# Kernel optimization log

Measured on AMD Instinct MI355X. Metric: run time of the kernel, lower is better.

Reference implementation:

```python
import jax, jax.numpy as jnp
import numpy as np

N = 100000          # num nodes
E = 1600000         # num edges (before self-loops)
IN = 128            # in_channels
HID = 32            # hidden_channels (= per-head dim, concat=False)
HEADS = 4
NEG_SLOPE = 0.2     # PyG GATConv default


def _glorot(k, shape):
    fan = shape[0] + shape[-1]
    return jax.random.normal(k, shape, jnp.float32) * np.float32(np.sqrt(2.0 / fan))


def setup_inputs() -> dict:
    key = jax.random.key(0)
    ks = jax.random.split(key, 18)
    inp = {}
    inp['x'] = jax.random.normal(ks[0], (N, IN), jnp.float32)
    inp['edge_index'] = jax.random.randint(ks[1], (2, E), 0, N, dtype=jnp.int64)
    dims_in = [IN, HID, HID]
    for i in range(3):
        inp[f'W{i+1}'] = _glorot(ks[2 + 4 * i], (dims_in[i], HEADS * HID))
        inp[f'as{i+1}'] = _glorot(ks[3 + 4 * i], (HEADS, HID))
        inp[f'ad{i+1}'] = _glorot(ks[4 + 4 * i], (HEADS, HID))
        inp[f'b{i+1}'] = jnp.zeros((HID,), jnp.float32)
    inp['lw1'] = _glorot(ks[14], (HID, HID // 2))
    inp['lb1'] = jnp.zeros((HID // 2,), jnp.float32)
    inp['lw2'] = _glorot(ks[15], (HID // 2, 1))
    inp['lb2'] = jnp.zeros((1,), jnp.float32)
    return inp


def gat_conv(x, src, dst, W, a_s, a_d, b):
    # x: [N, F_in]; src/dst: [E'] (self-loops included); concat=False -> head mean
    n = x.shape[0]
    h = (x @ W).reshape(n, HEADS, HID)                      # [N, H, C]
    alpha_src = jnp.einsum('nhc,hc->nh', h, a_s)            # [N, H]
    alpha_dst = jnp.einsum('nhc,hc->nh', h, a_d)            # [N, H]
    e = jax.nn.leaky_relu(alpha_src[src] + alpha_dst[dst], NEG_SLOPE)  # [E', H]
    # softmax over edges grouped by destination node
    e_max = jax.ops.segment_max(e, dst, num_segments=n)     # [N, H]
    e = jnp.exp(e - e_max[dst])
    denom = jax.ops.segment_sum(e, dst, num_segments=n)     # [N, H]
    alpha = e / (denom[dst] + 1e-16)                        # [E', H]
    msg = h[src] * alpha[:, :, None]                        # [E', H, C]
    out = jax.ops.segment_sum(msg, dst, num_segments=n)     # [N, H, C]
    return out.mean(axis=1) + b                             # concat=False: mean heads


def reference(x, edge_index, W1, as1, ad1, b1, W2, as2, ad2, b2, W3, as3, ad3, b3, lw1, lb1, lw2, lb2):
    # add self-loops (PyG GATConv default add_self_loops=True)
    loop = jnp.arange(N, dtype=edge_index.dtype)
    src = jnp.concatenate([edge_index[0], loop])
    dst = jnp.concatenate([edge_index[1], loop])
    h = jax.nn.relu(gat_conv(x, src, dst, W1, as1, ad1, b1))
    h = jax.nn.relu(gat_conv(h, src, dst, W2, as2, ad2, b2))
    h = jax.nn.relu(gat_conv(h, src, dst, W3, as3, ad3, b3))
    g = h.mean(axis=0, keepdims=True)                       # global_mean_pool, batch=None -> [1, HID]
    g = jax.nn.relu(g @ lw1 + lb1)                          # dropout is identity in eval
    return g @ lw2 + lb2                                    # [1, 1]
```

## Files before the change

### kernel.cpp

```cpp
#include <hip/hip_runtime.h>
#include <hip/hip_bf16.h>


#define HEADS 4
#define HID 32
#define F_HID 128
#define NEG_SLOPE 0.2f
#define BSHIFT 5
#define MAXB 3328
#define CAP 768
#define NSCAT 256

typedef float v2f __attribute__((ext_vector_type(2)));
using s8bf  = __attribute__((ext_vector_type(8))) short;
using f32x4 = __attribute__((ext_vector_type(4))) float;

__device__ __forceinline__ float lrelu(float v) { return v > 0.f ? v : NEG_SLOPE * v; }

__device__ __forceinline__ uint32_t bf16_rne(float f) {
    union { float f; uint32_t u; } c; c.f = f;
    return (c.u + 0x7fffu + ((c.u >> 16) & 1u)) >> 16;
}
__device__ __forceinline__ v2f up2(uint32_t u) {
    v2f r;
    r.x = __uint_as_float(u << 16);
    r.y = __uint_as_float(u & 0xffff0000u);
    return r;
}
__device__ __forceinline__ float bperm_f(int addr, float v) {
    return __int_as_float(__builtin_amdgcn_ds_bpermute(addr, __float_as_int(v)));
}
__device__ __forceinline__ int bperm_i(int addr, int v) {
    return __builtin_amdgcn_ds_bpermute(addr, v);
}
__device__ __forceinline__ v2f vshflxor(v2f v, int m) {
    v2f r; r.x = __shfl_xor(v.x, m); r.y = __shfl_xor(v.y, m); return r;
}


__device__ __forceinline__ void prep_one(const float* W, const float* a_s, const float* a_d,
                                         unsigned short* wbt, int FIN, int idx) {
    int LDK = FIN + 8;
    int r = idx / LDK, k = idx % LDK;
    float v = 0.f;
    if (k < FIN) {
        if (r < 128) {
            v = W[(size_t)k * F_HID + r];
        } else if (r < 136) {
            int j = r - 128;
            const float* av = (j < 4) ? a_s : a_d;
            int hd = j & 3;
            float s = 0.f;
            for (int c = 0; c < 32; c++)
                s += W[(size_t)k * F_HID + hd * 32 + c] * av[hd * 32 + c];
            v = s;
        }
    }
    wbt[idx] = (unsigned short)bf16_rne(v);
}

__global__ __launch_bounds__(256) void prep_all(const float* __restrict__ W1, const float* __restrict__ as1, const float* __restrict__ ad1,
                                                const float* __restrict__ W2, const float* __restrict__ as2, const float* __restrict__ ad2,
                                                const float* __restrict__ W3, const float* __restrict__ as3, const float* __restrict__ ad3,
                                                unsigned short* __restrict__ wbt1,
                                                unsigned short* __restrict__ wbt2,
                                                unsigned short* __restrict__ wbt3,
                                                int* __restrict__ gcursor, int nb,
                                                float* __restrict__ g) {
    int t = blockIdx.x * 256 + threadIdx.x;
    const int N1 = 144 * 136, N2 = 144 * 40, N3 = 144 * 40;
    if (t < N1) {
        prep_one(W1, as1, ad1, wbt1, 128, t);
    } else if (t < N1 + N2) {
        prep_one(W2, as2, ad2, wbt2, 32, t - N1);
    } else if (t < N1 + N2 + N3) {
        prep_one(W3, as3, ad3, wbt3, 32, t - N1 - N2);
    } else {
        int z = t - (N1 + N2 + N3);
        if (z < nb) gcursor[z] = z * CAP;
        else if (z < nb + 33) g[z - nb] = 0.f;
    }
}


__device__ void scatter_body(const int* __restrict__ ei, int E, int nb,
                             int* __restrict__ gcursor, uint32_t* __restrict__ tmp,
                             char* smem) {
    int* hist = (int*)smem;
    int* base = hist + MAXB;
    int t = threadIdx.x;
    int per = (E + NSCAT - 1) / NSCAT;
    int e0 = blockIdx.x * per;
    int e1 = e0 + per; if (e1 > E) e1 = E;

    for (int i = t; i < nb; i += 256) hist[i] = 0;
    __syncthreads();
    for (int i = e0 + t; i < e1; i += 256) {
        int d = ei[E + i];
        atomicAdd(&hist[d >> BSHIFT], 1);
    }
    __syncthreads();
    for (int i = t; i < nb; i += 256) {
        int c = hist[i];
        base[i] = c ? atomicAdd(&gcursor[i], c) : 0;
        hist[i] = 0;
    }
    __syncthreads();
    for (int i = e0 + t; i < e1; i += 256) {
        int d = ei[E + i];
        int s = ei[i];
        int b = d >> BSHIFT;
        int loc = atomicAdd(&hist[b], 1);
        tmp[base[b] + loc] = ((uint32_t)s << BSHIFT) | (uint32_t)(d & 31);
    }
}

template <int FIN>
__device__ void gemm_body(const float* __restrict__ x,
                          const unsigned short* __restrict__ wbt,
                          uint32_t* __restrict__ hb,
                          float* __restrict__ asrc,
                          float* __restrict__ adst, int n, int blk, char* smem) {
    constexpr int LDK = FIN + 8;
    constexpr int NPB = 64;
    unsigned short* xs = (unsigned short*)smem;
    int t = threadIdx.x;
    int base = blk * NPB;

    {
        constexpr int XIT = NPB * FIN / 4;
        for (int idx = t; idx < XIT; idx += 256) {
            int node = idx / (FIN / 4);
            int k4 = (idx % (FIN / 4)) * 4;
            int gnode = base + node;
            float4 v;
            if (gnode < n) v = *(const float4*)&x[(size_t)gnode * FIN + k4];
            else { v.x = 0.f; v.y = 0.f; v.z = 0.f; v.w = 0.f; }
            uint2 pk;
            pk.x = bf16_rne(v.x) | (bf16_rne(v.y) << 16);
            pk.y = bf16_rne(v.z) | (bf16_rne(v.w) << 16);
            *(uint2*)&xs[node * LDK + k4] = pk;
        }
    }
    __syncthreads();

    int w = t >> 6;
    int l = t & 63;
    int lr = l & 15, lg = l >> 4;
    int node = base + w * 16 + lr;
    const unsigned short* xrow = &xs[(w * 16 + lr) * LDK + lg * 8];

    for (int ct = 0; ct < 9; ct++) {
        f32x4 acc = {0.f, 0.f, 0.f, 0.f};
        const unsigned short* arow = wbt + (ct * 16 + lr) * LDK + lg * 8;
#pragma unroll
        for (int kt = 0; kt < FIN / 32; kt++) {
            s8bf a = *(const s8bf*)(arow + kt * 32);
            s8bf b = *(const s8bf*)(xrow + kt * 32);
            acc = __builtin_amdgcn_mfma_f32_16x16x32_bf16(a, b, acc, 0, 0, 0);
        }
        if (node < n) {
            if (ct < 8) {
                uint2 pp;
                pp.x = bf16_rne(acc[0]) | (bf16_rne(acc[1]) << 16);
                pp.y = bf16_rne(acc[2]) | (bf16_rne(acc[3]) << 16);
                *(uint2*)&hb[(size_t)node * 64 + ct * 8 + lg * 2] = pp;
            } else {
                float4 o; o.x = acc[0]; o.y = acc[1]; o.z = acc[2]; o.w = acc[3];
                if (lg == 0)      *(float4*)&asrc[node * 4] = o;
                else if (lg == 1) *(float4*)&adst[node * 4] = o;
            }
        }
    }
}

__global__ __launch_bounds__(256) void scatter_gemm1(const int* __restrict__ ei, int E, int nb,
                                                     int* __restrict__ gcursor,
                                                     uint32_t* __restrict__ tmp,
                                                     const float* __restrict__ x,
                                                     const unsigned short* __restrict__ wbt1,
                                                     uint32_t* __restrict__ hb,
                                                     float* __restrict__ asrc,
                                                     float* __restrict__ adst, int n) {
    __shared__ __align__(16) char smem[2 * MAXB * 4];
    if (blockIdx.x < NSCAT)
        scatter_body(ei, E, nb, gcursor, tmp, smem);
    else
        gemm_body<128>(x, wbt1, hb, asrc, adst, n, blockIdx.x - NSCAT, smem);
}

template <int FIN>
__global__ __launch_bounds__(256) void gemm_mfma(const float* __restrict__ x,
                                                 const unsigned short* __restrict__ wbt,
                                                 uint32_t* __restrict__ hb,
                                                 float* __restrict__ asrc,
                                                 float* __restrict__ adst, int n) {
    constexpr int LDK = FIN + 8;
    __shared__ __align__(16) char smem[64 * LDK * 2];
    gemm_body<FIN>(x, wbt, hb, asrc, adst, n, blockIdx.x, smem);
}

__global__ __launch_bounds__(256) void bucket_sort(uint32_t* __restrict__ tmp,
                                                   const int* __restrict__ gcursor,
                                                   int n,
                                                   int* __restrict__ row_start,
                                                   int* __restrict__ deg) {
    __shared__ uint32_t ebuf[CAP];
    __shared__ int cnt[32], pre[32];
    int b = blockIdx.x;
    int node0 = b << BSHIFT;
    int base = b * CAP;
    int cntE = gcursor[b] - base;
    int t = threadIdx.x;
    if (t < 32) cnt[t] = 0;
    __syncthreads();
    for (int i = t; i < cntE; i += 256) {
        uint32_t v = tmp[base + i];
        ebuf[i] = v;
        atomicAdd(&cnt[v & 31], 1);
    }
    __syncthreads();
    if (t == 0) {
        int run = 0;
        for (int i = 0; i < 32; i++) { pre[i] = run; run += cnt[i]; }
    }
    __syncthreads();
    if (t < 32) {
        int nd = node0 + t;
        if (nd < n) {
            row_start[nd] = base + pre[t];
            deg[nd] = cnt[t];
        }
        cnt[t] = pre[t];
    }
    __syncthreads();
    for (int i = t; i < cntE; i += 256) {
        uint32_t v = ebuf[i];
        int pos = atomicAdd(&cnt[v & 31], 1);
        tmp[base + pos] = v >> BSHIFT;
    }
}

__global__ __launch_bounds__(256) void aggregate(const uint32_t* __restrict__ hb,
                                                 const float* __restrict__ asrc,
                                                 const float* __restrict__ adst,
                                                 const int* __restrict__ row_start,
                                                 const int* __restrict__ deg,
                                                 const int* __restrict__ csr_src,
                                                 const float* __restrict__ bias,
                                                 float* __restrict__ xout, int n) {
    int d = blockIdx.x * 4 + (threadIdx.x >> 6);
    if (d >= n) return;
    int l = threadIdx.x & 63;
    int hd = l >> 4;
    int ci = l & 15;
    int hh = (l & 15) >> 2;
    int permH = hh << 6;
    int permb = permH + (l >> 4) * 4;
    int rowoff = hh * 64 + (l & 3) * 16;

    int start = row_start[d];
    int cnt = deg[d];
    float ad = adst[d * HEADS + hd];
    float e_self = lrelu(asrc[d * HEADS + hd] + ad);
    const char* hbbase = (const char*)hb;

    uint4 us = *(const uint4*)(hbbase + (((uint32_t)d) << 8) + rowoff);

    float dsum = 0.f;
    v2f a0 = {0.f, 0.f}, a1 = {0.f, 0.f}, a2 = {0.f, 0.f}, a3 = {0.f, 0.f};
    const int* csr = csr_src + start;

#define ACC4(U, PJ)                         \
    {                                       \
        v2f p2 = {PJ, PJ};                  \
        a0 += p2 * up2((U).x);              \
        a1 += p2 * up2((U).y);              \
        a2 += p2 * up2((U).z);              \
        a3 += p2 * up2((U).w);              \
    }

    for (int j0 = 0; j0 < cnt; j0 += 32) {
        int ncnt = cnt - j0; if (ncnt > 32) ncnt = 32;
        int jA = j0 + ci;      if (jA > cnt - 1) jA = cnt - 1;
        int jB = j0 + 16 + ci; if (jB > cnt - 1) jB = cnt - 1;
        int s0 = csr[jA];
        int s1 = csr[jB];

        int sj0 = bperm_i(permb,      s0);
        int sj1 = bperm_i(permb + 16, s0);
        int sj2 = bperm_i(permb + 32, s0);
        int sj3 = bperm_i(permb + 48, s0);
        int sj4 = bperm_i(permb,      s1);
        int sj5 = bperm_i(permb + 16, s1);
        int sj6 = bperm_i(permb + 32, s1);
        int sj7 = bperm_i(permb + 48, s1);
        uint4 u0 = *(const uint4*)(hbbase + (((uint32_t)sj0) << 8) + rowoff);
        uint4 u1 = *(const uint4*)(hbbase + (((uint32_t)sj1) << 8) + rowoff);
        uint4 u2 = *(const uint4*)(hbbase + (((uint32_t)sj2) << 8) + rowoff);
        uint4 u3 = *(const uint4*)(hbbase + (((uint32_t)sj3) << 8) + rowoff);
        uint4 u4 = *(const uint4*)(hbbase + (((uint32_t)sj4) << 8) + rowoff);
        uint4 u5 = *(const uint4*)(hbbase + (((uint32_t)sj5) << 8) + rowoff);
        uint4 u6 = *(const uint4*)(hbbase + (((uint32_t)sj6) << 8) + rowoff);
        uint4 u7 = *(const uint4*)(hbbase + (((uint32_t)sj7) << 8) + rowoff);

        float pe0 = (ci < ncnt)      ? __expf(lrelu(asrc[s0 * HEADS + hd] + ad)) : 0.f;
        float pe1 = (ci + 16 < ncnt) ? __expf(lrelu(asrc[s1 * HEADS + hd] + ad)) : 0.f;
        dsum += pe0 + pe1;
        float pj0 = bperm_f(permb,      pe0);
        float pj1 = bperm_f(permb + 16, pe0);
        float pj2 = bperm_f(permb + 32, pe0);
        float pj3 = bperm_f(permb + 48, pe0);
        float pj4 = bperm_f(permb,      pe1);
        float pj5 = bperm_f(permb + 16, pe1);
        float pj6 = bperm_f(permb + 32, pe1);
        float pj7 = bperm_f(permb + 48, pe1);

        ACC4(u0, pj0); ACC4(u1, pj1); ACC4(u2, pj2); ACC4(u3, pj3);
        ACC4(u4, pj4); ACC4(u5, pj5); ACC4(u6, pj6); ACC4(u7, pj7);
    }
#undef ACC4

    dsum += __shfl_xor(dsum, 8);
    dsum += __shfl_xor(dsum, 4);
    dsum += __shfl_xor(dsum, 2);
    dsum += __shfl_xor(dsum, 1);
    float ps = __expf(e_self);
    float inv = 1.f / (dsum + ps + 1e-16f);
    float psg = bperm_f(permH, ps);
    float invg = bperm_f(permH, inv);

    a0 += vshflxor(a0, 16); a0 += vshflxor(a0, 32);
    a1 += vshflxor(a1, 16); a1 += vshflxor(a1, 32);
    a2 += vshflxor(a2, 16); a2 += vshflxor(a2, 32);
    a3 += vshflxor(a3, 16); a3 += vshflxor(a3, 32);

    v2f ps2 = {psg, psg};
    a0 += ps2 * up2(us.x);
    a1 += ps2 * up2(us.y);
    a2 += ps2 * up2(us.z);
    a3 += ps2 * up2(us.w);
    v2f iv2 = {invg, invg};
    a0 *= iv2; a1 *= iv2; a2 *= iv2; a3 *= iv2;

    a0 += vshflxor(a0, 4); a0 += vshflxor(a0, 8);
    a1 += vshflxor(a1, 4); a1 += vshflxor(a1, 8);
    a2 += vshflxor(a2, 4); a2 += vshflxor(a2, 8);
    a3 += vshflxor(a3, 4); a3 += vshflxor(a3, 8);

    if (l < 4) {
        const float4* bv = (const float4*)&bias[l * 8];
        float4 b0 = bv[0], b1 = bv[1];
        float4 o0, o1;
        o0.x = 0.25f * a0.x + b0.x; o0.y = 0.25f * a0.y + b0.y;
        o0.z = 0.25f * a1.x + b0.z; o0.w = 0.25f * a1.y + b0.w;
        o1.x = 0.25f * a2.x + b1.x; o1.y = 0.25f * a2.y + b1.y;
        o1.z = 0.25f * a3.x + b1.z; o1.w = 0.25f * a3.y + b1.w;
        o0.x = o0.x > 0.f ? o0.x : 0.f;  o0.y = o0.y > 0.f ? o0.y : 0.f;
        o0.z = o0.z > 0.f ? o0.z : 0.f;  o0.w = o0.w > 0.f ? o0.w : 0.f;
        o1.x = o1.x > 0.f ? o1.x : 0.f;  o1.y = o1.y > 0.f ? o1.y : 0.f;
        o1.z = o1.z > 0.f ? o1.z : 0.f;  o1.w = o1.w > 0.f ? o1.w : 0.f;
        float4* op = (float4*)&xout[(size_t)d * HID + l * 8];
        op[0] = o0;
        op[1] = o1;
    }
}


__global__ __launch_bounds__(256) void pool_mlp(const float* __restrict__ x, int n,
                                                float* __restrict__ g,
                                                const float* __restrict__ lw1, const float* __restrict__ lb1,
                                                const float* __restrict__ lw2, const float* __restrict__ lb2,
                                                float* __restrict__ out, float invn) {
    __shared__ float sm[256];
    __shared__ int lastf;
    int t = threadIdx.x;
    int c = t & 31;
    int r = t >> 5;
    float acc = 0.f;
    for (int i = blockIdx.x * 8 + r; i < n; i += gridDim.x * 8)
        acc += x[(size_t)i * HID + c];
    sm[t] = acc;
    __syncthreads();
    if (t < 32) {
        float v = 0.f;
#pragma unroll
        for (int k = 0; k < 8; k++) v += sm[t + 32 * k];
        atomicAdd(&g[t], v);
    }
    __threadfence();
    if (t == 0) {
        int old = atomicAdd((int*)&g[32], 1);
        lastf = (old == (int)gridDim.x - 1) ? 1 : 0;
    }
    __syncthreads();
    if (!lastf) return;
    __threadfence();
    if (t < 32) sm[t] = atomicAdd(&g[t], 0.f) * invn;
    __syncthreads();
    float q = 0.f;
    if (t < 16) {
        q = lb1[t];
        for (int cc = 0; cc < 32; cc++) q += sm[cc] * lw1[cc * 16 + t];
        q = q > 0.f ? q : 0.f;
        q *= lw2[t];
    }
    if (t < 64) {
#pragma unroll
        for (int off = 8; off >= 1; off >>= 1) q += __shfl_xor(q, off);
        if (t == 0) out[0] = q + lb2[0];
    }
}


extern "C" void kernel_launch(void* const* d_in, const int* in_sizes, int n_in,
                              void* d_out, int out_size, void* d_ws, size_t ws_size,
                              hipStream_t stream) {
    const float* x   = (const float*)d_in[0];
    const int*   ei  = (const int*)d_in[1];
    const float* W1  = (const float*)d_in[2];
    const float* as1 = (const float*)d_in[3];
    const float* ad1 = (const float*)d_in[4];
    const float* b1  = (const float*)d_in[5];
    const float* W2  = (const float*)d_in[6];
    const float* as2 = (const float*)d_in[7];
    const float* ad2 = (const float*)d_in[8];
    const float* b2  = (const float*)d_in[9];
    const float* W3  = (const float*)d_in[10];
    const float* as3 = (const float*)d_in[11];
    const float* ad3 = (const float*)d_in[12];
    const float* b3  = (const float*)d_in[13];
    const float* lw1 = (const float*)d_in[14];
    const float* lb1 = (const float*)d_in[15];
    const float* lw2 = (const float*)d_in[16];
    const float* lb2 = (const float*)d_in[17];
    float* out = (float*)d_out;

    int n = in_sizes[0] / 128;
    int E = in_sizes[1] / 2;
    int nb = (n + 31) >> BSHIFT;

    char* p = (char*)d_ws;
    auto alloc = [&](size_t bytes) -> void* {
        void* r = (void*)p;
        p += (bytes + 255) & ~(size_t)255;
        return r;
    };
    int* deg       = (int*)alloc((size_t)n * 4);
    int* row_start = (int*)alloc((size_t)n * 4);
    int* gcursor   = (int*)alloc((size_t)nb * 4);
    uint32_t* tmp  = (uint32_t*)alloc((size_t)nb * CAP * 4);
    float* asrc    = (float*)alloc((size_t)n * HEADS * 4);
    float* adst    = (float*)alloc((size_t)n * HEADS * 4);
    uint32_t* hb   = (uint32_t*)alloc((size_t)n * 64 * 4);
    float* xA      = (float*)alloc((size_t)n * HID * 4);
    float* xB      = (float*)alloc((size_t)n * HID * 4);
    float* g       = (float*)alloc(33 * 4);
    unsigned short* wbt1 = (unsigned short*)alloc((size_t)144 * 136 * 2);
    unsigned short* wbt2 = (unsigned short*)alloc((size_t)144 * 40 * 2);
    unsigned short* wbt3 = (unsigned short*)alloc((size_t)144 * 40 * 2);

    int prep_tot = 144 * 136 + 2 * 144 * 40 + nb + 33;
    prep_all<<<(prep_tot + 255) / 256, 256, 0, stream>>>(
        W1, as1, ad1, W2, as2, ad2, W3, as3, ad3,
        wbt1, wbt2, wbt3, gcursor, nb, g);

    int gb = (n + 63) / 64;
    int ggb = (n + 3) / 4;

    scatter_gemm1<<<NSCAT + gb, 256, 0, stream>>>(ei, E, nb, gcursor, tmp,
                                                  x, wbt1, hb, asrc, adst, n);
    bucket_sort<<<nb, 256, 0, stream>>>(tmp, gcursor, n, row_start, deg);
    int* csr = (int*)tmp;

    aggregate<<<ggb, 256, 0, stream>>>(hb, asrc, adst, row_start, deg, csr, b1, xA, n);

    gemm_mfma<32><<<gb, 256, 0, stream>>>(xA, wbt2, hb, asrc, adst, n);
    aggregate<<<ggb, 256, 0, stream>>>(hb, asrc, adst, row_start, deg, csr, b2, xB, n);

    gemm_mfma<32><<<gb, 256, 0, stream>>>(xB, wbt3, hb, asrc, adst, n);
    aggregate<<<ggb, 256, 0, stream>>>(hb, asrc, adst, row_start, deg, csr, b3, xA, n);

    pool_mlp<<<256, 256, 0, stream>>>(xA, n, g, lw1, lb1, lw2, lb2, out, 1.0f / (float)n);
}
```

Measured before the change: 376.0 us.

## Split edge bucketing into two-pass radix partition by coarse then fine buckets

Replaces the single-pass scatter, which used a 3328-entry shared histogram per block, with a two-level partition. The first pass splits edges into about 49 coarse partitions of 2048 destinations inside the fused GEMM kernel, and a new partB kernel sub-buckets each partition into 64 fine buckets. The intent is to shrink the shared histogram, cut scattered global writes and global atomics, and lower shared memory use so the fused GEMM blocks get better occupancy. The cost is an extra kernel launch and one more full read and write of the edge list through an intermediate buffer.

```diff
diff --git a/kernel.cpp b/kernel.cpp
--- a/kernel.cpp
+++ b/kernel.cpp
@@ -7,9 +7,10 @@
 #define F_HID 128
 #define NEG_SLOPE 0.2f
 #define BSHIFT 5
-#define MAXB 3328
 #define CAP 768
-#define NSCAT 256
+#define NSCATA 256
+#define PSHIFT 11
+#define SLICE 8
 
 typedef float v2f __attribute__((ext_vector_type(2)));
 using s8bf  = __attribute__((ext_vector_type(8))) short;
@@ -66,6 +67,7 @@
                                                 unsigned short* __restrict__ wbt2,
                                                 unsigned short* __restrict__ wbt3,
                                                 int* __restrict__ gcursor, int nb,
+                                                int* __restrict__ pcursor, int P, int CAPP,
                                                 float* __restrict__ g) {
     int t = blockIdx.x * 256 + threadIdx.x;
     const int N1 = 144 * 136, N2 = 144 * 40, N3 = 144 * 40;
@@ -78,40 +80,39 @@
     } else {
         int z = t - (N1 + N2 + N3);
         if (z < nb) gcursor[z] = z * CAP;
-        else if (z < nb + 33) g[z - nb] = 0.f;
-    }
-}
-
-
-__device__ void scatter_body(const int* __restrict__ ei, int E, int nb,
-                             int* __restrict__ gcursor, uint32_t* __restrict__ tmp,
-                             char* smem) {
+        else if (z < nb + P) pcursor[z - nb] = (z - nb) * CAPP;
+        else if (z < nb + P + 33) g[z - nb - P] = 0.f;
+    }
+}
+
+
+__device__ void partA_body(const int* __restrict__ ei, int E, int P,
+                           int* __restrict__ pcursor, uint32_t* __restrict__ pbuf,
+                           char* smem) {
     int* hist = (int*)smem;
-    int* base = hist + MAXB;
+    int* base = hist + 64;
     int t = threadIdx.x;
-    int per = (E + NSCAT - 1) / NSCAT;
+    int per = (E + NSCATA - 1) / NSCATA;
     int e0 = blockIdx.x * per;
     int e1 = e0 + per; if (e1 > E) e1 = E;
 
-    for (int i = t; i < nb; i += 256) hist[i] = 0;
-    __syncthreads();
-    for (int i = e0 + t; i < e1; i += 256) {
-        int d = ei[E + i];
-        atomicAdd(&hist[d >> BSHIFT], 1);
-    }
-    __syncthreads();
-    for (int i = t; i < nb; i += 256) {
+    for (int i = t; i < P; i += 256) hist[i] = 0;
+    __syncthreads();
+    for (int i = e0 + t; i < e1; i += 256)
+        atomicAdd(&hist[ei[E + i] >> PSHIFT], 1);
+    __syncthreads();
+    for (int i = t; i < P; i += 256) {
         int c = hist[i];
-        base[i] = c ? atomicAdd(&gcursor[i], c) : 0;
+        base[i] = c ? atomicAdd(&pcursor[i], c) : 0;
         hist[i] = 0;
     }
     __syncthreads();
     for (int i = e0 + t; i < e1; i += 256) {
         int d = ei[E + i];
         int s = ei[i];
-        int b = d >> BSHIFT;
-        int loc = atomicAdd(&hist[b], 1);
-        tmp[base[b] + loc] = ((uint32_t)s << BSHIFT) | (uint32_t)(d & 31);
+        int p = d >> PSHIFT;
+        int loc = atomicAdd(&hist[p], 1);
+        pbuf[base[p] + loc] = ((uint32_t)s << PSHIFT) | (uint32_t)(d & ((1 << PSHIFT) - 1));
     }
 }
 
@@ -174,19 +175,54 @@
     }
 }
 
-__global__ __launch_bounds__(256) void scatter_gemm1(const int* __restrict__ ei, int E, int nb,
-                                                     int* __restrict__ gcursor,
-                                                     uint32_t* __restrict__ tmp,
+__global__ __launch_bounds__(256) void scatter_gemm1(const int* __restrict__ ei, int E, int P,
+                                                     int* __restrict__ pcursor,
+                                                     uint32_t* __restrict__ pbuf,
                                                      const float* __restrict__ x,
                                                      const unsigned short* __restrict__ wbt1,
                                                      uint32_t* __restrict__ hb,
                                                      float* __restrict__ asrc,
                                                      float* __restrict__ adst, int n) {
-    __shared__ __align__(16) char smem[2 * MAXB * 4];
-    if (blockIdx.x < NSCAT)
-        scatter_body(ei, E, nb, gcursor, tmp, smem);
+    __shared__ __align__(16) char smem[64 * 136 * 2];
+    if (blockIdx.x < NSCATA)
+        partA_body(ei, E, P, pcursor, pbuf, smem);
     else
-        gemm_body<128>(x, wbt1, hb, asrc, adst, n, blockIdx.x - NSCAT, smem);
+        gemm_body<128>(x, wbt1, hb, asrc, adst, n, blockIdx.x - NSCATA, smem);
+}
+
+__global__ __launch_bounds__(256) void partB(const uint32_t* __restrict__ pbuf,
+                                             const int* __restrict__ pcursor,
+                                             int CAPP,
+                                             int* __restrict__ gcursor,
+                                             uint32_t* __restrict__ tmp) {
+    __shared__ int hist[64], base[64];
+    int p = blockIdx.x / SLICE;
+    int sl = blockIdx.x % SLICE;
+    int pbase = p * CAPP;
+    int pcnt = pcursor[p] - pbase;
+    int per = (pcnt + SLICE - 1) / SLICE;
+    int e0 = sl * per;
+    int e1 = e0 + per; if (e1 > pcnt) e1 = pcnt;
+    int t = threadIdx.x;
+    if (t < 64) hist[t] = 0;
+    __syncthreads();
+    for (int i = e0 + t; i < e1; i += 256)
+        atomicAdd(&hist[(pbuf[pbase + i] & ((1 << PSHIFT) - 1)) >> BSHIFT], 1);
+    __syncthreads();
+    if (t < 64) {
+        int c = hist[t];
+        base[t] = c ? atomicAdd(&gcursor[p * 64 + t], c) : 0;
+        hist[t] = 0;
+    }
+    __syncthreads();
+    for (int i = e0 + t; i < e1; i += 256) {
+        uint32_t v = pbuf[pbase + i];
+        uint32_t s = v >> PSHIFT;
+        uint32_t dlo = v & ((1 << PSHIFT) - 1);
+        int lb = dlo >> BSHIFT;
+        int loc = atomicAdd(&hist[lb], 1);
+        tmp[base[lb] + loc] = (s << BSHIFT) | (dlo & 31);
+    }
 }
 
 template <int FIN>
@@ -439,6 +475,9 @@
     int n = in_sizes[0] / 128;
     int E = in_sizes[1] / 2;
     int nb = (n + 31) >> BSHIFT;
+    int P  = (n + (1 << PSHIFT) - 1) >> PSHIFT;
+    int CAPP = (E + P - 1) / P;
+    CAPP = CAPP + (CAPP >> 2) + 256;
 
     char* p = (char*)d_ws;
     auto alloc = [&](size_t bytes) -> void* {
@@ -449,6 +488,8 @@
     int* deg       = (int*)alloc((size_t)n * 4);
     int* row_start = (int*)alloc((size_t)n * 4);
     int* gcursor   = (int*)alloc((size_t)nb * 4);
+    int* pcursor   = (int*)alloc((size_t)P * 4);
+    uint32_t* pbuf = (uint32_t*)alloc((size_t)P * CAPP * 4);
     uint32_t* tmp  = (uint32_t*)alloc((size_t)nb * CAP * 4);
     float* asrc    = (float*)alloc((size_t)n * HEADS * 4);
     float* adst    = (float*)alloc((size_t)n * HEADS * 4);
@@ -460,16 +501,17 @@
     unsigned short* wbt2 = (unsigned short*)alloc((size_t)144 * 40 * 2);
     unsigned short* wbt3 = (unsigned short*)alloc((size_t)144 * 40 * 2);
 
-    int prep_tot = 144 * 136 + 2 * 144 * 40 + nb + 33;
+    int prep_tot = 144 * 136 + 2 * 144 * 40 + nb + P + 33;
     prep_all<<<(prep_tot + 255) / 256, 256, 0, stream>>>(
         W1, as1, ad1, W2, as2, ad2, W3, as3, ad3,
-        wbt1, wbt2, wbt3, gcursor, nb, g);
+        wbt1, wbt2, wbt3, gcursor, nb, pcursor, P, CAPP, g);
 
     int gb = (n + 63) / 64;
     int ggb = (n + 3) / 4;
 
-    scatter_gemm1<<<NSCAT + gb, 256, 0, stream>>>(ei, E, nb, gcursor, tmp,
-                                                  x, wbt1, hb, asrc, adst, n);
+    scatter_gemm1<<<NSCATA + gb, 256, 0, stream>>>(ei, E, P, pcursor, pbuf,
+                                                   x, wbt1, hb, asrc, adst, n);
+    partB<<<P * SLICE, 256, 0, stream>>>(pbuf, pcursor, CAPP, gcursor, tmp);
     bucket_sort<<<nb, 256, 0, stream>>>(tmp, gcursor, n, row_start, deg);
     int* csr = (int*)tmp;
 
```

Result: no change. 382.0 us (+1.6%).
